# Kernel optimization log

Hardware: AMD Instinct MI355X
Metric: run time of the kernel (lower is better)

The kernel has to match this reference:

```python
import jax, jax.numpy as jnp
import numpy as np

N_NODES = 100000


def gcn_conv(h, row, col, deg_inv_sqrt, W, b, n_nodes):
    # h: [N, F_in]; PyG GCNConv: linear first, then normalized scatter-add aggregation
    h = h @ W  # [N, F_out]
    norm = deg_inv_sqrt[row] * deg_inv_sqrt[col]  # [E']
    msg = h[row] * norm[:, None]  # gather + scale, [E', F_out]
    out = jax.ops.segment_sum(msg, col, num_segments=n_nodes)  # scatter-add
    return out + b


def setup_inputs() -> dict:
    key = jax.random.key(0)
    ks = jax.random.split(key, 8)
    x = jax.random.normal(ks[0], (N_NODES, 1), dtype=jnp.float32)
    edge_index = jax.random.randint(ks[1], (2, 3200000), 0, N_NODES, dtype=jnp.int64)
    W1 = jax.random.normal(ks[2], (1, 64), dtype=jnp.float32) * 0.5
    b1 = jax.random.normal(ks[3], (64,), dtype=jnp.float32) * 0.1
    W2 = jax.random.normal(ks[4], (64, 32), dtype=jnp.float32) * 0.125
    b2 = jax.random.normal(ks[5], (32,), dtype=jnp.float32) * 0.1
    W3 = jax.random.normal(ks[6], (32, 1), dtype=jnp.float32) * 0.18
    b3 = jax.random.normal(ks[7], (1,), dtype=jnp.float32) * 0.1
    return {"x": x, "edge_index": edge_index, "W1": W1, "b1": b1,
            "W2": W2, "b2": b2, "W3": W3, "b3": b3}


def reference(x, edge_index, W1, b1, W2, b2, W3, b3):
    n = x.shape[0]
    # add self-loops (PyG GCNConv default)
    loops = jnp.arange(n, dtype=edge_index.dtype)
    row = jnp.concatenate([edge_index[0], loops])  # source
    col = jnp.concatenate([edge_index[1], loops])  # target
    # symmetric normalization: deg computed on target nodes with unit edge weight
    deg = jax.ops.segment_sum(jnp.ones_like(col, dtype=x.dtype), col, num_segments=n)
    deg_inv_sqrt = jnp.where(deg > 0, jax.lax.rsqrt(deg), 0.0)

    h = jax.nn.relu(gcn_conv(x, row, col, deg_inv_sqrt, W1, b1, n))
    h = jax.nn.relu(gcn_conv(h, row, col, deg_inv_sqrt, W2, b2, n))
    h = gcn_conv(h, row, col, deg_inv_sqrt, W3, b3, n)  # [N, 1]
    return jax.nn.sigmoid(jnp.sum(h, axis=0))  # [1]
```

## Files before the change

kernel.cpp:

```cpp
#include <hip/hip_runtime.h>
#include <math.h>


#define TB 256
#define TBC 1024
#define TBS 512
#define NPB 128
#define NBMAX 1024
#define CHUNK 8192
#define NCHMAX 512
#define CAPB 6144
#define P8SCALE 64.0f
#define P8INV (1.0f / 64.0f)
#define RMASK 0x1FFFFu

__device__ inline int block_scan_incl(int v, int t, int nthreads, int* wsums) {
#pragma unroll
    for (int d = 1; d < 64; d <<= 1) {
        int n = __shfl_up(v, d);
        if ((t & 63) >= d) v += n;
    }
    int wid = t >> 6;
    if ((t & 63) == 63) wsums[wid] = v;
    __syncthreads();
    if (wid == 0) {
        int nw = nthreads >> 6;
        int s = (t < nw) ? wsums[t] : 0;
#pragma unroll
        for (int d = 1; d < 16; d <<= 1) {
            int n = __shfl_up(s, d);
            if (t >= d) s += n;
        }
        if (t < nw) wsums[t] = s;
    }
    __syncthreads();
    if (wid > 0) v += wsums[wid - 1];
    return v;
}

__global__ void k_init(const int* __restrict__ ei, int* __restrict__ flag,
                       int* __restrict__ tot, int NB, float* __restrict__ accum) {
    __shared__ int any_nonzero;
    int t = threadIdx.x;
    if (t == 0) any_nonzero = 0;
    __syncthreads();
    if (t < 128) {
        if (ei[2 * t + 1] != 0) atomicOr(&any_nonzero, 1);
    }
    __syncthreads();
    if (t == 0) { flag[0] = (any_nonzero == 0) ? 1 : 0; accum[0] = 0.f; }
    for (int i = t; i < NB; i += blockDim.x) tot[i] = 0;
}

__global__ __launch_bounds__(TBC) void k_chunksort(
        const int* __restrict__ ei, int E, const int* __restrict__ flag,
        unsigned* __restrict__ sbin, unsigned short* __restrict__ s16,
        int* __restrict__ tot, int NB, int nstride) {
    __shared__ int hist[NBMAX];
    __shared__ int cur[NBMAX];
    __shared__ unsigned stage[CHUNK];
    __shared__ int wsums[TBC / 64];
    int t = threadIdx.x;
    int sh = flag[0];
    int c0 = blockIdx.x * CHUNK;
    int c1 = min(c0 + CHUNK, E);
    int n = c1 - c0;
    for (int i = t; i < NB; i += TBC) hist[i] = 0;
    __syncthreads();
    for (int e = c0 + t; e < c1; e += TBC) {
        int c = ei[(size_t)(E + e) << sh];
        atomicAdd(&hist[c >> 7], 1);
    }
    __syncthreads();
    int v = (t < NB) ? hist[t] : 0;
    int incl = block_scan_incl(v, t, TBC, wsums);
    int excl = incl - v;
    cur[t] = excl;
    if (t < NB) {
        s16[(size_t)blockIdx.x * nstride + t] = (unsigned short)excl;
        if (v) atomicAdd(&tot[t], v);
    }
    if (t == 0) s16[(size_t)blockIdx.x * nstride + NB] = (unsigned short)n;
    __syncthreads();
    for (int e = c0 + t; e < c1; e += TBC) {
        int r = ei[(size_t)e << sh];
        int c = ei[(size_t)(E + e) << sh];
        int rank = atomicAdd(&cur[c >> 7], 1);
        stage[rank] = ((unsigned)(c & 127) << 17) | (unsigned)r;
    }
    __syncthreads();
    unsigned* dst = sbin + (size_t)blockIdx.x * CHUNK;
    for (int i = t; i < n; i += TBC) dst[i] = stage[i];
}

__global__ void k_scanbins(const int* __restrict__ tot, int* __restrict__ binoff,
                           int NB, int E) {
    __shared__ int wsums[1024 / 64];
    int t = threadIdx.x;
    int v = (t < NB) ? tot[t] : 0;
    int incl = block_scan_incl(v, t, 1024, wsums);
    if (t < NB) binoff[t] = incl - v;
    if (t == 0) binoff[NB] = E;
}

__global__ __launch_bounds__(TBS) void k_binsort(
        const unsigned* __restrict__ sbin, const unsigned short* __restrict__ s16,
        const int* __restrict__ binoff, unsigned* __restrict__ srow,
        int* __restrict__ off, int* __restrict__ deg,
        const float* __restrict__ x, float* __restrict__ dis,
        float* __restrict__ y, int N, int nchunk, int nstride) {
    __shared__ unsigned stage[CAPB];
    __shared__ int hist[NPB];
    __shared__ int wsums[TBS / 64];
    int b = blockIdx.x, t = threadIdx.x;
    int b0 = b << 7;
    int nn = min(NPB, N - b0);
    int s0v = 0, v = 0;
    if (t < nchunk) {
        s0v = (int)s16[(size_t)t * nstride + b];
        v = (int)s16[(size_t)t * nstride + b + 1] - s0v;
    }
    int incl = block_scan_incl(v, t, TBS, wsums);
    int myexcl = incl - v;
    if (t < nchunk && v > 0 && myexcl < CAPB) {
        int vc = min(v, CAPB - myexcl);
        const unsigned* src = sbin + (size_t)t * CHUNK + s0v;
        for (int i = 0; i < vc; ++i) stage[myexcl + i] = src[i];
    }
    int bo = binoff[b];
    int cntE = min(binoff[b + 1] - bo, CAPB);
    if (t < NPB) hist[t] = 0;
    __syncthreads();
    for (int i = t; i < cntE; i += TBS) atomicAdd(&hist[stage[i] >> 17], 1);
    __syncthreads();
    int hv = (t < NPB) ? hist[t] : 0;
    int hincl = block_scan_incl(hv, t, TBS, wsums);
    int nexcl = hincl - hv;
    if (t < nn) {
        int node = b0 + t;
        off[node] = bo + nexcl;
        deg[node] = hv;
        float dd = rsqrtf((float)(hv + 1));
        dis[node] = dd;
        y[node] = x[node] * dd;
    }
    __syncthreads();
    if (t < NPB) hist[t] = nexcl;
    __syncthreads();
    for (int i = t; i < cntE; i += TBS) {
        unsigned pk = stage[i];
        int rank = atomicAdd(&hist[pk >> 17], 1);
        srow[bo + rank] = pk;
    }
}

__global__ __launch_bounds__(TB) void k_layer1(
        const int* __restrict__ off, const int* __restrict__ deg,
        const unsigned* __restrict__ srow, const float* __restrict__ y,
        const float* __restrict__ dis,
        const float* __restrict__ W1, const float* __restrict__ b1,
        const float* __restrict__ W2, unsigned* __restrict__ p8, int N) {
    __shared__ float sW1[64], sb1[64];
    __shared__ float4 sW2[512];
    for (int k = threadIdx.x; k < 64; k += TB) { sW1[k] = W1[k]; sb1[k] = b1[k]; }
    const float4* W2v = (const float4*)W2;
    for (int k = threadIdx.x; k < 512; k += TB) sW2[k] = W2v[k];
    __syncthreads();

    int c = blockIdx.x * TB + threadIdx.x;
    if (c >= N) return;
    int k0 = off[c], nd = deg[c];
    float ss[8];
#pragma unroll
    for (int j = 0; j < 8; ++j) ss[j] = 0.f;
    int k = 0;
    for (; k + 8 <= nd; k += 8) {
        unsigned rr[8];
#pragma unroll
        for (int j = 0; j < 8; ++j) rr[j] = srow[k0 + k + j] & RMASK;
#pragma unroll
        for (int j = 0; j < 8; ++j) ss[j] += y[rr[j]];
    }
    for (; k < nd; ++k) ss[0] += y[srow[k0 + k] & RMASK];
    float d = dis[c];
    float s_ = (((ss[0] + ss[1]) + (ss[2] + ss[3])) +
                ((ss[4] + ss[5]) + (ss[6] + ss[7])) + y[c]) * d;

    float4 g[8];
#pragma unroll
    for (int jj = 0; jj < 8; ++jj) g[jj] = make_float4(0.f, 0.f, 0.f, 0.f);
    for (int f = 0; f < 64; ++f) {
        float hf = fmaxf(fmaf(s_, sW1[f], sb1[f]), 0.f);
#pragma unroll
        for (int jj = 0; jj < 8; ++jj) {
            float4 w = sW2[f * 8 + jj];
            g[jj].x = fmaf(hf, w.x, g[jj].x);
            g[jj].y = fmaf(hf, w.y, g[jj].y);
            g[jj].z = fmaf(hf, w.z, g[jj].z);
            g[jj].w = fmaf(hf, w.w, g[jj].w);
        }
    }
    float sc = d * P8SCALE;
    unsigned pk[8];
#pragma unroll
    for (int jj = 0; jj < 8; ++jj) {
        unsigned u = 0;
        u = __builtin_amdgcn_cvt_pk_fp8_f32(g[jj].x * sc, g[jj].y * sc, u, false);
        u = __builtin_amdgcn_cvt_pk_fp8_f32(g[jj].z * sc, g[jj].w * sc, u, true);
        pk[jj] = u;
    }
    uint4* pv = (uint4*)&p8[(size_t)c * 8];
    pv[0] = make_uint4(pk[0], pk[1], pk[2], pk[3]);
    pv[1] = make_uint4(pk[4], pk[5], pk[6], pk[7]);
}

__global__ __launch_bounds__(TB) void k_layer2(
        const int* __restrict__ off, const int* __restrict__ deg,
        const unsigned* __restrict__ srow, const unsigned* __restrict__ p8,
        const float* __restrict__ dis, const float* __restrict__ b2,
        const float* __restrict__ W3, float* __restrict__ q, int N) {
    int w = (blockIdx.x * TB + threadIdx.x) >> 6;
    int lane = threadIdx.x & 63;
    int grp = lane >> 3;
    int l8 = lane & 7;
    float a0 = 0.f, a1 = 0.f, a2 = 0.f, a3 = 0.f;
    if (w < N) {
        int k0 = off[w], nd = deg[w];
        for (int base = 0; base < nd; base += 64) {
            int m = min(64, nd - base);
            int idx = 0;
            if (lane < m) idx = (int)srow[k0 + base + lane];
            int rr[8];
            unsigned vv[8];
#pragma unroll
            for (int j = 0; j < 8; ++j)
                rr[j] = __shfl(idx, grp + 8 * j) & RMASK;
#pragma unroll
            for (int j = 0; j < 8; ++j)
                vv[j] = (grp + 8 * j < m) ? p8[(size_t)rr[j] * 8 + l8] : 0u;
#pragma unroll
            for (int j = 0; j < 8; ++j) {
                auto lo = __builtin_amdgcn_cvt_pk_f32_fp8(vv[j], false);
                auto hi = __builtin_amdgcn_cvt_pk_f32_fp8(vv[j], true);
                a0 += lo[0]; a1 += lo[1]; a2 += hi[0]; a3 += hi[1];
            }
        }
    }
    a0 += __shfl_down(a0, 32); a1 += __shfl_down(a1, 32);
    a2 += __shfl_down(a2, 32); a3 += __shfl_down(a3, 32);
    a0 += __shfl_down(a0, 16); a1 += __shfl_down(a1, 16);
    a2 += __shfl_down(a2, 16); a3 += __shfl_down(a3, 16);
    a0 += __shfl_down(a0, 8);  a1 += __shfl_down(a1, 8);
    a2 += __shfl_down(a2, 8);  a3 += __shfl_down(a3, 8);
    float prod = 0.f;
    float d = (w < N) ? dis[w] : 0.f;
    if (w < N && lane < 8) {
        unsigned v = p8[(size_t)w * 8 + l8];
        auto lo = __builtin_amdgcn_cvt_pk_f32_fp8(v, false);
        auto hi = __builtin_amdgcn_cvt_pk_f32_fp8(v, true);
        float4 b2v = ((const float4*)b2)[l8];
        float4 w3v = ((const float4*)W3)[l8];
        float z0 = fmaf(d, (a0 + lo[0]) * P8INV, b2v.x);
        float z1 = fmaf(d, (a1 + lo[1]) * P8INV, b2v.y);
        float z2 = fmaf(d, (a2 + hi[0]) * P8INV, b2v.z);
        float z3 = fmaf(d, (a3 + hi[1]) * P8INV, b2v.w);
        prod = fmaxf(z0, 0.f) * w3v.x + fmaxf(z1, 0.f) * w3v.y
             + fmaxf(z2, 0.f) * w3v.z + fmaxf(z3, 0.f) * w3v.w;
    }
    prod += __shfl_down(prod, 4);
    prod += __shfl_down(prod, 2);
    prod += __shfl_down(prod, 1);
    if (w < N && lane == 0) q[w] = prod * d;
}

__global__ __launch_bounds__(TB) void k_final(
        const unsigned* __restrict__ srow, const int* __restrict__ binoff,
        const float* __restrict__ q, const float* __restrict__ dis,
        int N, float* __restrict__ accum) {
    __shared__ float red[TB / 64];
    int b = blockIdx.x, t = threadIdx.x;
    int b0 = b << 7;
    int s0 = binoff[b], s1 = binoff[b + 1];
    float acc = 0.f;
    for (int i = s0 + t; i < s1; i += TB) {
        unsigned pk = srow[i];
        acc = fmaf(q[pk & RMASK], dis[b0 + (pk >> 17)], acc);
    }
    int node = b0 + t;
    if (t < NPB && node < N) acc = fmaf(dis[node], q[node], acc);
    acc += __shfl_down(acc, 32); acc += __shfl_down(acc, 16);
    acc += __shfl_down(acc, 8);  acc += __shfl_down(acc, 4);
    acc += __shfl_down(acc, 2);  acc += __shfl_down(acc, 1);
    int lane = t & 63;
    if (lane == 0) red[t >> 6] = acc;
    __syncthreads();
    if (t == 0)
        atomicAdd(accum, red[0] + red[1] + red[2] + red[3]);
}

__global__ void k_out(const float* __restrict__ accum, const float* __restrict__ b3,
                      float* __restrict__ out, float Nf) {
    float z = accum[0] + Nf * b3[0];
    out[0] = 1.f / (1.f + expf(-z));
}

extern "C" void kernel_launch(void* const* d_in, const int* in_sizes, int n_in,
                              void* d_out, int out_size, void* d_ws, size_t ws_size,
                              hipStream_t stream) {
    const float* x  = (const float*)d_in[0];
    const int*   ei = (const int*)d_in[1];
    const float* W1 = (const float*)d_in[2];
    const float* b1 = (const float*)d_in[3];
    const float* W2 = (const float*)d_in[4];
    const float* b2 = (const float*)d_in[5];
    const float* W3 = (const float*)d_in[6];
    const float* b3 = (const float*)d_in[7];
    float* out = (float*)d_out;

    const int N = in_sizes[0];
    const int E = in_sizes[1] / 2;
    if (N > (1 << 17)) return;
    const int NB = (N + NPB - 1) >> 7;
    const int nchunk = (E + CHUNK - 1) / CHUNK;
    const int nstride = NB + 1;
    if (NB > NBMAX || nchunk > NCHMAX || nchunk > TBS) return;

    char* w = (char*)d_ws;
    size_t o = 0;
    auto alloc = [&](size_t bytes) -> void* {
        void* ptr = w + o;
        o += (bytes + 255) & ~(size_t)255;
        return ptr;
    };
    int*            flag   = (int*)     alloc(256);
    float*          accum  = (float*)   alloc(256);
    int*            tot    = (int*)     alloc((size_t)NBMAX * 4);
    int*            binoff = (int*)     alloc((size_t)(NBMAX + 1) * 4);
    int*            off    = (int*)     alloc((size_t)N * 4);
    int*            deg    = (int*)     alloc((size_t)N * 4);
    float*          dis    = (float*)   alloc((size_t)N * 4);
    float*          y      = (float*)   alloc((size_t)N * 4);
    float*          q      = (float*)   alloc((size_t)N * 4);
    unsigned*       sbin   = (unsigned*)alloc((size_t)nchunk * CHUNK * 4);
    unsigned short* s16    = (unsigned short*)alloc((size_t)nchunk * nstride * 2);
    unsigned*       srow   = (unsigned*)alloc(((size_t)E + 64) * 4);
    unsigned*       p8     = (unsigned*)alloc((size_t)N * 32);
    if (o > ws_size) return;

    const int nbN = (N + TB - 1) / TB;
    const int nbWave = (N * 64 + TB - 1) / TB;

    k_init<<<1, 1024, 0, stream>>>(ei, flag, tot, NB, accum);
    k_chunksort<<<nchunk, TBC, 0, stream>>>(ei, E, flag, sbin, s16, tot, NB, nstride);
    k_scanbins<<<1, 1024, 0, stream>>>(tot, binoff, NB, E);
    k_binsort<<<NB, TBS, 0, stream>>>(sbin, s16, binoff, srow, off, deg, x, dis, y, N, nchunk, nstride);
    k_layer1<<<nbN, TB, 0, stream>>>(off, deg, srow, y, dis, W1, b1, W2, p8, N);
    k_layer2<<<nbWave, TB, 0, stream>>>(off, deg, srow, p8, dis, b2, W3, q, N);
    k_final<<<NB, TB, 0, stream>>>(srow, binoff, q, dis, N, accum);
    k_out<<<1, 1, 0, stream>>>(accum, b3, out, (float)N);
}
```

Measured before the change: 153.4 us.

## Register-cache edges in chunk sort and widen fp8 gathers to 8-byte loads

The chunk sort kernel now loads each edge's row and column once into registers (8 per thread) during the histogram pass and reuses them for the scatter, instead of reading edge_index from global memory twice. It also reuses the hist array as the cursor array, dropping one shared array. The layer-2 aggregation now gathers each neighbour's 32 fp8 features with 4 lanes doing uint2 loads rather than 8 lanes doing 32-bit loads. That processes 16 neighbours per wave step instead of 8, at the cost of more accumulator registers and an extra shuffle-reduction level.

```diff
diff --git a/kernel.cpp b/kernel.cpp
--- a/kernel.cpp
+++ b/kernel.cpp
@@ -8,6 +8,7 @@
 #define NPB 128
 #define NBMAX 1024
 #define CHUNK 8192
+#define EPT 8
 #define NCHMAX 512
 #define CAPB 6144
 #define P8SCALE 64.0f
@@ -57,7 +58,6 @@
         unsigned* __restrict__ sbin, unsigned short* __restrict__ s16,
         int* __restrict__ tot, int NB, int nstride) {
     __shared__ int hist[NBMAX];
-    __shared__ int cur[NBMAX];
     __shared__ unsigned stage[CHUNK];
     __shared__ int wsums[TBC / 64];
     int t = threadIdx.x;
@@ -67,26 +67,41 @@
     int n = c1 - c0;
     for (int i = t; i < NB; i += TBC) hist[i] = 0;
     __syncthreads();
-    for (int e = c0 + t; e < c1; e += TBC) {
-        int c = ei[(size_t)(E + e) << sh];
-        atomicAdd(&hist[c >> 7], 1);
+    int rr[EPT], cc[EPT];
+#pragma unroll
+    for (int k = 0; k < EPT; ++k) {
+        int e = c0 + t + k * TBC;
+        int r = 0, c = -1;
+        if (e < c1) {
+            if (sh) {
+                r = ei[(size_t)e << 1];
+                c = ei[(size_t)(E + e) << 1];
+            } else {
+                r = ei[e];
+                c = ei[E + e];
+            }
+            atomicAdd(&hist[c >> 7], 1);
+        }
+        rr[k] = r; cc[k] = c;
     }
     __syncthreads();
     int v = (t < NB) ? hist[t] : 0;
     int incl = block_scan_incl(v, t, TBC, wsums);
     int excl = incl - v;
-    cur[t] = excl;
     if (t < NB) {
         s16[(size_t)blockIdx.x * nstride + t] = (unsigned short)excl;
         if (v) atomicAdd(&tot[t], v);
     }
     if (t == 0) s16[(size_t)blockIdx.x * nstride + NB] = (unsigned short)n;
     __syncthreads();
-    for (int e = c0 + t; e < c1; e += TBC) {
-        int r = ei[(size_t)e << sh];
-        int c = ei[(size_t)(E + e) << sh];
-        int rank = atomicAdd(&cur[c >> 7], 1);
-        stage[rank] = ((unsigned)(c & 127) << 17) | (unsigned)r;
+    hist[t] = excl;
+    __syncthreads();
+#pragma unroll
+    for (int k = 0; k < EPT; ++k) {
+        if (cc[k] >= 0) {
+            int rank = atomicAdd(&hist[cc[k] >> 7], 1);
+            stage[rank] = ((unsigned)(cc[k] & 127) << 17) | (unsigned)rr[k];
+        }
     }
     __syncthreads();
     unsigned* dst = sbin + (size_t)blockIdx.x * CHUNK;
@@ -221,53 +236,68 @@
         const float* __restrict__ W3, float* __restrict__ q, int N) {
     int w = (blockIdx.x * TB + threadIdx.x) >> 6;
     int lane = threadIdx.x & 63;
-    int grp = lane >> 3;
-    int l8 = lane & 7;
-    float a0 = 0.f, a1 = 0.f, a2 = 0.f, a3 = 0.f;
+    int grp = lane >> 2;
+    int l4 = lane & 3;
+    const uint2* p8v = (const uint2*)p8;
+    float a[8];
+#pragma unroll
+    for (int k = 0; k < 8; ++k) a[k] = 0.f;
     if (w < N) {
         int k0 = off[w], nd = deg[w];
         for (int base = 0; base < nd; base += 64) {
             int m = min(64, nd - base);
             int idx = 0;
             if (lane < m) idx = (int)srow[k0 + base + lane];
-            int rr[8];
-            unsigned vv[8];
-#pragma unroll
-            for (int j = 0; j < 8; ++j)
-                rr[j] = __shfl(idx, grp + 8 * j) & RMASK;
-#pragma unroll
-            for (int j = 0; j < 8; ++j)
-                vv[j] = (grp + 8 * j < m) ? p8[(size_t)rr[j] * 8 + l8] : 0u;
-#pragma unroll
-            for (int j = 0; j < 8; ++j) {
-                auto lo = __builtin_amdgcn_cvt_pk_f32_fp8(vv[j], false);
-                auto hi = __builtin_amdgcn_cvt_pk_f32_fp8(vv[j], true);
-                a0 += lo[0]; a1 += lo[1]; a2 += hi[0]; a3 += hi[1];
+            int rr[4];
+            uint2 vv[4];
+#pragma unroll
+            for (int j = 0; j < 4; ++j)
+                rr[j] = __shfl(idx, grp + 16 * j) & RMASK;
+#pragma unroll
+            for (int j = 0; j < 4; ++j) {
+                vv[j] = make_uint2(0u, 0u);
+                if (grp + 16 * j < m) vv[j] = p8v[(size_t)rr[j] * 4 + l4];
             }
-        }
-    }
-    a0 += __shfl_down(a0, 32); a1 += __shfl_down(a1, 32);
-    a2 += __shfl_down(a2, 32); a3 += __shfl_down(a3, 32);
-    a0 += __shfl_down(a0, 16); a1 += __shfl_down(a1, 16);
-    a2 += __shfl_down(a2, 16); a3 += __shfl_down(a3, 16);
-    a0 += __shfl_down(a0, 8);  a1 += __shfl_down(a1, 8);
-    a2 += __shfl_down(a2, 8);  a3 += __shfl_down(a3, 8);
+#pragma unroll
+            for (int j = 0; j < 4; ++j) {
+                auto lo0 = __builtin_amdgcn_cvt_pk_f32_fp8(vv[j].x, false);
+                auto hi0 = __builtin_amdgcn_cvt_pk_f32_fp8(vv[j].x, true);
+                auto lo1 = __builtin_amdgcn_cvt_pk_f32_fp8(vv[j].y, false);
+                auto hi1 = __builtin_amdgcn_cvt_pk_f32_fp8(vv[j].y, true);
+                a[0] += lo0[0]; a[1] += lo0[1]; a[2] += hi0[0]; a[3] += hi0[1];
+                a[4] += lo1[0]; a[5] += lo1[1]; a[6] += hi1[0]; a[7] += hi1[1];
+            }
+        }
+    }
+#pragma unroll
+    for (int k = 0; k < 8; ++k) {
+        a[k] += __shfl_down(a[k], 32);
+        a[k] += __shfl_down(a[k], 16);
+        a[k] += __shfl_down(a[k], 8);
+        a[k] += __shfl_down(a[k], 4);
+    }
     float prod = 0.f;
     float d = (w < N) ? dis[w] : 0.f;
-    if (w < N && lane < 8) {
-        unsigned v = p8[(size_t)w * 8 + l8];
-        auto lo = __builtin_amdgcn_cvt_pk_f32_fp8(v, false);
-        auto hi = __builtin_amdgcn_cvt_pk_f32_fp8(v, true);
-        float4 b2v = ((const float4*)b2)[l8];
-        float4 w3v = ((const float4*)W3)[l8];
-        float z0 = fmaf(d, (a0 + lo[0]) * P8INV, b2v.x);
-        float z1 = fmaf(d, (a1 + lo[1]) * P8INV, b2v.y);
-        float z2 = fmaf(d, (a2 + hi[0]) * P8INV, b2v.z);
-        float z3 = fmaf(d, (a3 + hi[1]) * P8INV, b2v.w);
-        prod = fmaxf(z0, 0.f) * w3v.x + fmaxf(z1, 0.f) * w3v.y
-             + fmaxf(z2, 0.f) * w3v.z + fmaxf(z3, 0.f) * w3v.w;
-    }
-    prod += __shfl_down(prod, 4);
+    if (w < N && lane < 4) {
+        uint2 sv = p8v[(size_t)w * 4 + l4];
+        auto lo0 = __builtin_amdgcn_cvt_pk_f32_fp8(sv.x, false);
+        auto hi0 = __builtin_amdgcn_cvt_pk_f32_fp8(sv.x, true);
+        auto lo1 = __builtin_amdgcn_cvt_pk_f32_fp8(sv.y, false);
+        auto hi1 = __builtin_amdgcn_cvt_pk_f32_fp8(sv.y, true);
+        float s[8] = {lo0[0], lo0[1], hi0[0], hi0[1],
+                      lo1[0], lo1[1], hi1[0], hi1[1]};
+        float4 b2a = ((const float4*)b2)[2 * l4];
+        float4 b2b = ((const float4*)b2)[2 * l4 + 1];
+        float4 w3a = ((const float4*)W3)[2 * l4];
+        float4 w3b = ((const float4*)W3)[2 * l4 + 1];
+        float bb[8] = {b2a.x, b2a.y, b2a.z, b2a.w, b2b.x, b2b.y, b2b.z, b2b.w};
+        float ww[8] = {w3a.x, w3a.y, w3a.z, w3a.w, w3b.x, w3b.y, w3b.z, w3b.w};
+#pragma unroll
+        for (int k = 0; k < 8; ++k) {
+            float z = fmaf(d, (a[k] + s[k]) * P8INV, bb[k]);
+            prod = fmaf(fmaxf(z, 0.f), ww[k], prod);
+        }
+    }
     prod += __shfl_down(prod, 2);
     prod += __shfl_down(prod, 1);
     if (w < N && lane == 0) q[w] = prod * d;
```

Result: slower. 160.7 us (+4.7%).
